# Kernel optimization log

Measured on AMD Instinct MI355X. Metric: run time of the kernel, lower is better.

## Reference

```python
import jax, jax.numpy as jnp
import numpy as np

N = 100_000   # nodes
E = 3_200_000 # edges (avg degree 32)
D = 128       # feature dim
L = 3         # encoder layers (GIN convs)
K = 2         # MLP linear layers per GIN conv (channel_list [128,128,128])
G = 64        # graphs in batch
C = 4         # output classes
BN_EPS = 1e-5


def setup_inputs() -> dict:
    key = jax.random.key(0)
    ks = jax.random.split(key, 12)
    x = jax.random.normal(ks[0], (N, D), dtype=jnp.float32)
    edge_index = jax.random.randint(ks[1], (2, E), 0, N, dtype=jnp.int64)
    batch = jnp.sort(jax.random.randint(ks[2], (N,), 0, G, dtype=jnp.int64))
    # GIN MLP params: L convs x K linear layers each, all D->D
    Ws = jax.random.normal(ks[3], (L, K, D, D), dtype=jnp.float32) * 0.05
    bs = jax.random.normal(ks[4], (L, K, D), dtype=jnp.float32) * 0.02
    # BatchNorm (eval mode) params/buffers per MLP layer
    gammas = 1.0 + 0.1 * jax.random.normal(ks[5], (L, K, D), dtype=jnp.float32)
    betas = 0.1 * jax.random.normal(ks[6], (L, K, D), dtype=jnp.float32)
    run_means = 0.1 * jax.random.normal(ks[7], (L, K, D), dtype=jnp.float32)
    run_vars = jax.random.uniform(ks[8], (L, K, D), dtype=jnp.float32, minval=0.5, maxval=1.5)
    # final classifier
    lin_W = jax.random.normal(ks[9], (D, C), dtype=jnp.float32) * 0.05
    lin_b = jax.random.normal(ks[10], (C,), dtype=jnp.float32) * 0.02
    return {"x": x, "edge_index": edge_index, "batch": batch,
            "Ws": Ws, "bs": bs, "gammas": gammas, "betas": betas,
            "run_means": run_means, "run_vars": run_vars,
            "lin_W": lin_W, "lin_b": lin_b}


def reference(x, edge_index, batch, Ws, bs, gammas, betas, run_means, run_vars, lin_W, lin_b):
    src, dst = edge_index[0], edge_index[1]
    h = x
    for l in range(L):
        # GINConv (eps=0): h_i <- MLP(h_i + sum_{j->i} h_j)
        agg = jax.ops.segment_sum(h[src], dst, num_segments=N)  # [N, D]
        h = h + agg
        for k in range(K):
            # Linear -> BatchNorm(eval) -> ReLU (plain_last=False, dropout=0)
            y = h @ Ws[l, k] + bs[l, k]
            scale = gammas[l, k] / jnp.sqrt(run_vars[l, k] + BN_EPS)
            h = jax.nn.relu((y - run_means[l, k]) * scale + betas[l, k])
    pooled = jax.ops.segment_max(h, batch, num_segments=G)  # [G, D]
    logits = pooled @ lin_W + lin_b                          # [G, C]
    return jax.nn.log_softmax(logits, axis=-1)
```

## Files before the change

### kernel.cpp

```cpp
#include <hip/hip_runtime.h>
#include <stdint.h>

#define NN 100000
#define EE 3200000
#define DD 128
#define GG 64
#define CC 4
#define LLAYERS 3
#define KLIN 2
#define BN_EPS 1e-5f

#define BSH 8
#define NB ((NN + 255) >> BSH)
#define CHUNK3 8192
#define NBLK3 ((EE + CHUNK3 - 1) / CHUNK3)
#define STAGE_CAP 10240

#define HSP 136

typedef unsigned short u16;
typedef unsigned int u32;
typedef short bf16x8 __attribute__((ext_vector_type(8)));
typedef float f32x4 __attribute__((ext_vector_type(4)));

__device__ __forceinline__ float bflo(u32 u){ return __uint_as_float(u << 16); }
__device__ __forceinline__ float bfhi(u32 u){ return __uint_as_float(u & 0xffff0000u); }
__device__ __forceinline__ u16 f2bf(float f){
  u32 u = __float_as_uint(f);
  u32 r = u + 0x7fffu + ((u >> 16) & 1u);
  return (u16)(r >> 16);
}


__global__ __launch_bounds__(256) void bucket_hist(const int* __restrict__ dst,
                                                   int* __restrict__ bcount){
  __shared__ int lh[NB];
  for (int i = threadIdx.x; i < NB; i += 256) lh[i] = 0;
  __syncthreads();
  int b0 = blockIdx.x * CHUNK3;
  int bend = min(b0 + CHUNK3, EE);
  for (int i = b0 + threadIdx.x; i < bend; i += 256)
    atomicAdd(&lh[dst[i] >> BSH], 1);
  __syncthreads();
  for (int i = threadIdx.x; i < NB; i += 256)
    if (lh[i]) atomicAdd(&bcount[i], lh[i]);
}

__global__ __launch_bounds__(512) void bucket_scan(const int* __restrict__ bcount,
                                                   int* __restrict__ bofs,
                                                   int* __restrict__ gcur,
                                                   int* __restrict__ row_start){
  __shared__ int s[512];
  int t = threadIdx.x;
  int v = (t < NB) ? bcount[t] : 0;
  s[t] = v; __syncthreads();
  for (int off = 1; off < 512; off <<= 1) {
    int u = (t >= off) ? s[t - off] : 0;
    __syncthreads();
    s[t] += u;
    __syncthreads();
  }
  if (t < NB) { int e = s[t] - v; bofs[t] = e; gcur[t] = e; }
  if (t == 0) row_start[NN] = EE;
}

__global__ __launch_bounds__(256) void bucket_scatter(const int* __restrict__ src,
                                                      const int* __restrict__ dst,
                                                      int* __restrict__ gcur,
                                                      int2* __restrict__ rec){
  __shared__ int lh[NB];
  __shared__ int lbase[NB];
  int b0 = blockIdx.x * CHUNK3;
  int bend = min(b0 + CHUNK3, EE);
  for (int i = threadIdx.x; i < NB; i += 256) lh[i] = 0;
  __syncthreads();
  for (int i = b0 + threadIdx.x; i < bend; i += 256)
    atomicAdd(&lh[dst[i] >> BSH], 1);
  __syncthreads();
  for (int i = threadIdx.x; i < NB; i += 256) {
    int c = lh[i];
    lbase[i] = c ? atomicAdd(&gcur[i], c) : 0;
    lh[i] = 0;
  }
  __syncthreads();
  for (int i = b0 + threadIdx.x; i < bend; i += 256) {
    int d = dst[i];
    int bk = d >> BSH;
    int pos = lbase[bk] + atomicAdd(&lh[bk], 1);
    rec[pos] = make_int2(src[i], d & ((1 << BSH) - 1));
  }
}

__global__ __launch_bounds__(256) void bucket_emit(const int2* __restrict__ rec,
                                                   const int* __restrict__ bofs,
                                                   const int* __restrict__ bcount,
                                                   int* __restrict__ row_start,
                                                   int* __restrict__ sorted_src){
  __shared__ int cnt[256];
  __shared__ int ofs[256];
  __shared__ int stage[STAGE_CAP];
  const int b = blockIdx.x, t = threadIdx.x;
  const int nodebase = b << BSH;
  const int nlocal = min(256, NN - nodebase);
  const int ebeg = bofs[b];
  const int ecnt = bcount[b];
  cnt[t] = 0;
  __syncthreads();
  for (int i = t; i < ecnt; i += 256) {
    int2 r = rec[ebeg + i];
    atomicAdd(&cnt[r.y], 1);
  }
  __syncthreads();
  int v = cnt[t];
  ofs[t] = v;
  __syncthreads();
  for (int off = 1; off < 256; off <<= 1) {
    int u = (t >= off) ? ofs[t - off] : 0;
    __syncthreads();
    ofs[t] += u;
    __syncthreads();
  }
  int excl = ofs[t] - v;
  if (t < nlocal) row_start[nodebase + t] = ebeg + excl;
  cnt[t] = excl;
  __syncthreads();
  for (int i = t; i < ecnt; i += 256) {
    int2 r = rec[ebeg + i];
    int pos = atomicAdd(&cnt[r.y], 1);
    if (pos < STAGE_CAP) stage[pos] = r.x;
    else sorted_src[ebeg + pos] = r.x;
  }
  __syncthreads();
  int lim = min(ecnt, STAGE_CAP);
  for (int i = t; i < lim; i += 256)
    sorted_src[ebeg + i] = stage[i];
}

__global__ __launch_bounds__(256) void prep_kernel(const float* __restrict__ Ws,
    const float* __restrict__ bs, const float* __restrict__ gammas,
    const float* __restrict__ betas, const float* __restrict__ means,
    const float* __restrict__ vars,
    u16* __restrict__ Wt6, float* __restrict__ scale6, float* __restrict__ shift6){
  const int s = blockIdx.x;
  const float* W = Ws + (size_t)s * DD * DD;
  u16* Wt = Wt6 + (size_t)s * DD * DD;
  const int t = threadIdx.x;
  if (t < DD) {
    float sc = gammas[s*DD+t] * rsqrtf(vars[s*DD+t] + BN_EPS);
    scale6[s*DD+t] = sc;
    shift6[s*DD+t] = (bs[s*DD+t] - means[s*DD+t]) * sc + betas[s*DD+t];
  }
  for (int f = t; f < DD*DD; f += 256) {
    int j = f & 7, lane = (f >> 3) & 63, ks = (f >> 9) & 3, ct = f >> 11;
    int k = ks*32 + (lane >> 4)*8 + j;
    int n = ct*16 + (lane & 15);
    Wt[f] = f2bf(W[k*DD + n]);
  }
}

__global__ __launch_bounds__(256) void cast_x_kernel(const float4* __restrict__ x,
                                                     uint4* __restrict__ h){
  int i = blockIdx.x * 256 + threadIdx.x;
  if (i < NN*DD/8) {
    float4 a = x[2*i], b = x[2*i+1];
    uint4 o;
    o.x = (u32)f2bf(a.x) | ((u32)f2bf(a.y) << 16);
    o.y = (u32)f2bf(a.z) | ((u32)f2bf(a.w) << 16);
    o.z = (u32)f2bf(b.x) | ((u32)f2bf(b.y) << 16);
    o.w = (u32)f2bf(b.z) | ((u32)f2bf(b.w) << 16);
    h[i] = o;
  }
}

__global__ __launch_bounds__(256) void gin_layer(
    const u16* __restrict__ H, u16* __restrict__ O,
    const int* __restrict__ row_start, const int* __restrict__ sorted_src,
    const u16* __restrict__ W1t, const float* __restrict__ scale1, const float* __restrict__ shift1,
    const u16* __restrict__ W2t, const float* __restrict__ scale2, const float* __restrict__ shift2)
{
  __shared__ u16 HS[16][HSP];
  __shared__ u16 YS[16][HSP];

  const int tid = threadIdx.x;
  const int base = blockIdx.x * 16;
  const uint4* hp = (const uint4*)H;

  {
    const int g = tid >> 4, l16 = tid & 15;
    const int node = base + g;
    uint4 v = hp[(size_t)node*16 + l16];
    float a0=bflo(v.x), a1=bfhi(v.x), a2=bflo(v.y), a3=bfhi(v.y);
    float a4=bflo(v.z), a5=bfhi(v.z), a6=bflo(v.w), a7=bfhi(v.w);
    float b0=0.f,b1=0.f,b2=0.f,b3=0.f,b4=0.f,b5=0.f,b6=0.f,b7=0.f;
    float c0=0.f,c1=0.f,c2=0.f,c3=0.f,c4=0.f,c5=0.f,c6=0.f,c7=0.f;
    float d0=0.f,d1=0.f,d2=0.f,d3=0.f,d4=0.f,d5=0.f,d6=0.f,d7=0.f;
    int e = row_start[node];
    const int end = row_start[node + 1];
    for (; e + 3 < end; e += 4) {
      int s0 = sorted_src[e],   s1 = sorted_src[e+1];
      int s2 = sorted_src[e+2], s3 = sorted_src[e+3];
      uint4 u0 = hp[(size_t)s0*16 + l16];
      uint4 u1 = hp[(size_t)s1*16 + l16];
      uint4 u2 = hp[(size_t)s2*16 + l16];
      uint4 u3 = hp[(size_t)s3*16 + l16];
      a0 += bflo(u0.x); a1 += bfhi(u0.x); a2 += bflo(u0.y); a3 += bfhi(u0.y);
      a4 += bflo(u0.z); a5 += bfhi(u0.z); a6 += bflo(u0.w); a7 += bfhi(u0.w);
      b0 += bflo(u1.x); b1 += bfhi(u1.x); b2 += bflo(u1.y); b3 += bfhi(u1.y);
      b4 += bflo(u1.z); b5 += bfhi(u1.z); b6 += bflo(u1.w); b7 += bfhi(u1.w);
      c0 += bflo(u2.x); c1 += bfhi(u2.x); c2 += bflo(u2.y); c3 += bfhi(u2.y);
      c4 += bflo(u2.z); c5 += bfhi(u2.z); c6 += bflo(u2.w); c7 += bfhi(u2.w);
      d0 += bflo(u3.x); d1 += bfhi(u3.x); d2 += bflo(u3.y); d3 += bfhi(u3.y);
      d4 += bflo(u3.z); d5 += bfhi(u3.z); d6 += bflo(u3.w); d7 += bfhi(u3.w);
    }
    for (; e < end; ++e) {
      int s0 = sorted_src[e];
      uint4 u0 = hp[(size_t)s0*16 + l16];
      a0 += bflo(u0.x); a1 += bfhi(u0.x); a2 += bflo(u0.y); a3 += bfhi(u0.y);
      a4 += bflo(u0.z); a5 += bfhi(u0.z); a6 += bflo(u0.w); a7 += bfhi(u0.w);
    }
    a0 += b0+c0+d0; a1 += b1+c1+d1; a2 += b2+c2+d2; a3 += b3+c3+d3;
    a4 += b4+c4+d4; a5 += b5+c5+d5; a6 += b6+c6+d6; a7 += b7+c7+d7;
    uint4 w;
    w.x = (u32)f2bf(a0) | ((u32)f2bf(a1) << 16);
    w.y = (u32)f2bf(a2) | ((u32)f2bf(a3) << 16);
    w.z = (u32)f2bf(a4) | ((u32)f2bf(a5) << 16);
    w.w = (u32)f2bf(a6) | ((u32)f2bf(a7) << 16);
    *(uint4*)&HS[g][l16*8] = w;
  }
  __syncthreads();

  const int wave = tid >> 6, lane = tid & 63;
  const int ln15 = lane & 15, quad = lane >> 4;

  {
    bf16x8 af[4];
    #pragma unroll
    for (int ks = 0; ks < 4; ++ks)
      af[ks] = *(const bf16x8*)&HS[ln15][ks*32 + quad*8];
    f32x4 acc[2];
    acc[0] = (f32x4){0.f,0.f,0.f,0.f};
    acc[1] = (f32x4){0.f,0.f,0.f,0.f};
    #pragma unroll
    for (int ks = 0; ks < 4; ++ks) {
      #pragma unroll
      for (int j = 0; j < 2; ++j) {
        const int ct = wave*2 + j;
        bf16x8 bf = *(const bf16x8*)(W1t + (((ct*4 + ks)*64 + lane) << 3));
        acc[j] = __builtin_amdgcn_mfma_f32_16x16x32_bf16(af[ks], bf, acc[j], 0, 0, 0);
      }
    }
    #pragma unroll
    for (int j = 0; j < 2; ++j) {
      const int col = (wave*2 + j)*16 + ln15;
      const float sc = scale1[col], sh = shift1[col];
      #pragma unroll
      for (int reg = 0; reg < 4; ++reg)
        YS[quad*4 + reg][col] = f2bf(fmaxf(acc[j][reg]*sc + sh, 0.f));
    }
  }
  __syncthreads();

  {
    bf16x8 af[4];
    #pragma unroll
    for (int ks = 0; ks < 4; ++ks)
      af[ks] = *(const bf16x8*)&YS[ln15][ks*32 + quad*8];
    f32x4 acc[2];
    acc[0] = (f32x4){0.f,0.f,0.f,0.f};
    acc[1] = (f32x4){0.f,0.f,0.f,0.f};
    #pragma unroll
    for (int ks = 0; ks < 4; ++ks) {
      #pragma unroll
      for (int j = 0; j < 2; ++j) {
        const int ct = wave*2 + j;
        bf16x8 bf = *(const bf16x8*)(W2t + (((ct*4 + ks)*64 + lane) << 3));
        acc[j] = __builtin_amdgcn_mfma_f32_16x16x32_bf16(af[ks], bf, acc[j], 0, 0, 0);
      }
    }
    #pragma unroll
    for (int j = 0; j < 2; ++j) {
      const int col = (wave*2 + j)*16 + ln15;
      const float sc = scale2[col], sh = shift2[col];
      #pragma unroll
      for (int reg = 0; reg < 4; ++reg) {
        const int row = base + quad*4 + reg;
        O[(size_t)row * DD + col] = f2bf(fmaxf(acc[j][reg]*sc + sh, 0.f));
      }
    }
  }
}

__global__ __launch_bounds__(256) void pool_seg_bf16(const u16* __restrict__ h,
    const int* __restrict__ batch, float* __restrict__ pooled){
  __shared__ float red[256 * 8];
  __shared__ int range[2];
  const int g = blockIdx.x, tid = threadIdx.x;
  if (tid < 2) {
    int target = g + tid;
    int lo = 0, hi = NN;
    while (lo < hi) { int mid = (lo + hi) >> 1; if (batch[mid] < target) lo = mid + 1; else hi = mid; }
    range[tid] = lo;
  }
  __syncthreads();
  const int beg = range[0], end = range[1];
  const int rg = tid >> 4, l16 = tid & 15;
  const uint4* hp = (const uint4*)h;
  float m0=0.f,m1=0.f,m2=0.f,m3=0.f,m4=0.f,m5=0.f,m6=0.f,m7=0.f;
  for (int n = beg + rg; n < end; n += 16) {
    uint4 u = hp[(size_t)n * 16 + l16];
    m0 = fmaxf(m0, bflo(u.x)); m1 = fmaxf(m1, bfhi(u.x));
    m2 = fmaxf(m2, bflo(u.y)); m3 = fmaxf(m3, bfhi(u.y));
    m4 = fmaxf(m4, bflo(u.z)); m5 = fmaxf(m5, bfhi(u.z));
    m6 = fmaxf(m6, bflo(u.w)); m7 = fmaxf(m7, bfhi(u.w));
  }
  float* r = &red[tid * 8];
  r[0]=m0; r[1]=m1; r[2]=m2; r[3]=m3; r[4]=m4; r[5]=m5; r[6]=m6; r[7]=m7;
  __syncthreads();
  #pragma unroll
  for (int off = 8; off > 0; off >>= 1) {
    if (rg < off) {
      float* o = &red[(tid + off*16) * 8];
      #pragma unroll
      for (int i = 0; i < 8; ++i) r[i] = fmaxf(r[i], o[i]);
    }
    __syncthreads();
  }
  if (rg == 0) {
    #pragma unroll
    for (int i = 0; i < 8; ++i) pooled[g*DD + l16*8 + i] = r[i];
  }
}

__global__ __launch_bounds__(64) void classify_kernel(const float* __restrict__ pooled,
    const float* __restrict__ lw, const float* __restrict__ lb, float* __restrict__ out){
  int g = blockIdx.x, lane = threadIdx.x;
  float x0 = pooled[g*DD + lane];
  float x1 = pooled[g*DD + 64 + lane];
  float4 wA = *(const float4*)(lw + lane*4);
  float4 wB = *(const float4*)(lw + (lane+64)*4);
  float a0 = x0*wA.x + x1*wB.x;
  float a1 = x0*wA.y + x1*wB.y;
  float a2 = x0*wA.z + x1*wB.z;
  float a3 = x0*wA.w + x1*wB.w;
  #pragma unroll
  for (int off = 32; off > 0; off >>= 1) {
    a0 += __shfl_down(a0, off);
    a1 += __shfl_down(a1, off);
    a2 += __shfl_down(a2, off);
    a3 += __shfl_down(a3, off);
  }
  if (lane == 0) {
    float l0 = a0 + lb[0];
    float l1 = a1 + lb[1];
    float l2 = a2 + lb[2];
    float l3 = a3 + lb[3];
    float m = fmaxf(fmaxf(l0,l1), fmaxf(l2,l3));
    float s = expf(l0-m)+expf(l1-m)+expf(l2-m)+expf(l3-m);
    float lse = logf(s) + m;
    out[g*4+0] = l0 - lse;
    out[g*4+1] = l1 - lse;
    out[g*4+2] = l2 - lse;
    out[g*4+3] = l3 - lse;
  }
}

extern "C" void kernel_launch(void* const* d_in, const int* in_sizes, int n_in,
                              void* d_out, int out_size, void* d_ws, size_t ws_size,
                              hipStream_t stream) {
  const float* x     = (const float*)d_in[0];
  const int* ei      = (const int*)d_in[1];
  const int* batch   = (const int*)d_in[2];
  const float* Ws    = (const float*)d_in[3];
  const float* bs    = (const float*)d_in[4];
  const float* gammas= (const float*)d_in[5];
  const float* betas = (const float*)d_in[6];
  const float* means = (const float*)d_in[7];
  const float* vars  = (const float*)d_in[8];
  const float* lw    = (const float*)d_in[9];
  const float* lb    = (const float*)d_in[10];
  float* out = (float*)d_out;

  u16* hA = (u16*)d_ws;
  u16* hB = hA + (size_t)NN * DD;
  float* pooled = (float*)(hB + (size_t)NN * DD);
  float* scale6 = pooled + GG * DD;
  float* shift6 = scale6 + 6 * DD;
  int* row_start  = (int*)(shift6 + 6 * DD);
  int* bcount     = row_start + NN + 2;
  int* bofs       = bcount + NB;
  int* gcur       = bofs + NB;
  int* sorted_src = gcur + NB + 3;
  u16* Wt6 = (u16*)(((uintptr_t)(sorted_src + EE) + 63) & ~(uintptr_t)63);
  int2* rec = (int2*)hA;

  const int* srcIdx = ei;
  const int* dstIdx = ei + EE;

  hipMemsetAsync(bcount, 0, NB * sizeof(int), stream);
  bucket_hist<<<NBLK3, 256, 0, stream>>>(dstIdx, bcount);
  bucket_scan<<<1, 512, 0, stream>>>(bcount, bofs, gcur, row_start);
  bucket_scatter<<<NBLK3, 256, 0, stream>>>(srcIdx, dstIdx, gcur, rec);
  bucket_emit<<<NB, 256, 0, stream>>>(rec, bofs, bcount, row_start, sorted_src);

  prep_kernel<<<6, 256, 0, stream>>>(Ws, bs, gammas, betas, means, vars,
                                     Wt6, scale6, shift6);
  cast_x_kernel<<<(NN*DD/8 + 255)/256, 256, 0, stream>>>((const float4*)x, (uint4*)hA);

  u16* cur = hA;
  u16* tmp = hB;
  const int layer_grid = NN / 16;
  for (int l = 0; l < LLAYERS; ++l) {
    int s0 = l*KLIN + 0, s1 = l*KLIN + 1;
    gin_layer<<<layer_grid, 256, 0, stream>>>(cur, tmp, row_start, sorted_src,
        Wt6 + (size_t)s0*DD*DD, scale6 + s0*DD, shift6 + s0*DD,
        Wt6 + (size_t)s1*DD*DD, scale6 + s1*DD, shift6 + s1*DD);
    u16* t = cur; cur = tmp; tmp = t;
  }

  pool_seg_bf16<<<GG, 256, 0, stream>>>(cur, batch, pooled);
  classify_kernel<<<GG, 64, 0, stream>>>(pooled, lw, lb, out);
}
```

Baseline: 650.4 us.

## Pack edge records, vectorize bucketing loads, fuse prep/cast and pool/classify

Edge records in the bucketing sort are packed from an int2 into a single u32 (src shifted left by 8, local dst in the low byte), halving the rec traffic in scatter and emit. The histogram and scatter loops now read src and dst as int4 vectors. The weight-prep and x-cast kernels are merged into one launch, and segment-max pooling is fused with the classifier, which removes two launches and the pooled buffer. Packing assumes src fits in 24 bits, which holds for N=100000.

```diff
diff --git a/kernel.cpp b/kernel.cpp
--- a/kernel.cpp
+++ b/kernel.cpp
@@ -37,10 +37,19 @@
   __shared__ int lh[NB];
   for (int i = threadIdx.x; i < NB; i += 256) lh[i] = 0;
   __syncthreads();
-  int b0 = blockIdx.x * CHUNK3;
-  int bend = min(b0 + CHUNK3, EE);
-  for (int i = b0 + threadIdx.x; i < bend; i += 256)
-    atomicAdd(&lh[dst[i] >> BSH], 1);
+  const int b0 = blockIdx.x * CHUNK3;
+  const int cnt = min(CHUNK3, EE - b0);
+  const int4* d4 = (const int4*)(dst + b0);
+  const int n4 = cnt >> 2;
+  for (int i = threadIdx.x; i < n4; i += 256) {
+    int4 v = d4[i];
+    atomicAdd(&lh[v.x >> BSH], 1);
+    atomicAdd(&lh[v.y >> BSH], 1);
+    atomicAdd(&lh[v.z >> BSH], 1);
+    atomicAdd(&lh[v.w >> BSH], 1);
+  }
+  for (int i = (n4 << 2) + threadIdx.x; i < cnt; i += 256)
+    atomicAdd(&lh[dst[b0 + i] >> BSH], 1);
   __syncthreads();
   for (int i = threadIdx.x; i < NB; i += 256)
     if (lh[i]) atomicAdd(&bcount[i], lh[i]);
@@ -67,15 +76,25 @@
 __global__ __launch_bounds__(256) void bucket_scatter(const int* __restrict__ src,
                                                       const int* __restrict__ dst,
                                                       int* __restrict__ gcur,
-                                                      int2* __restrict__ rec){
+                                                      u32* __restrict__ rec){
   __shared__ int lh[NB];
   __shared__ int lbase[NB];
-  int b0 = blockIdx.x * CHUNK3;
-  int bend = min(b0 + CHUNK3, EE);
+  const int b0 = blockIdx.x * CHUNK3;
+  const int cnt = min(CHUNK3, EE - b0);
+  const int n4 = cnt >> 2;
+  const int4* s4 = (const int4*)(src + b0);
+  const int4* d4 = (const int4*)(dst + b0);
   for (int i = threadIdx.x; i < NB; i += 256) lh[i] = 0;
   __syncthreads();
-  for (int i = b0 + threadIdx.x; i < bend; i += 256)
-    atomicAdd(&lh[dst[i] >> BSH], 1);
+  for (int i = threadIdx.x; i < n4; i += 256) {
+    int4 v = d4[i];
+    atomicAdd(&lh[v.x >> BSH], 1);
+    atomicAdd(&lh[v.y >> BSH], 1);
+    atomicAdd(&lh[v.z >> BSH], 1);
+    atomicAdd(&lh[v.w >> BSH], 1);
+  }
+  for (int i = (n4 << 2) + threadIdx.x; i < cnt; i += 256)
+    atomicAdd(&lh[dst[b0 + i] >> BSH], 1);
   __syncthreads();
   for (int i = threadIdx.x; i < NB; i += 256) {
     int c = lh[i];
@@ -83,15 +102,38 @@
     lh[i] = 0;
   }
   __syncthreads();
-  for (int i = b0 + threadIdx.x; i < bend; i += 256) {
-    int d = dst[i];
+  for (int i = threadIdx.x; i < n4; i += 256) {
+    int4 ss = s4[i], dd = d4[i];
+    {
+      int bk = dd.x >> BSH;
+      int pos = lbase[bk] + atomicAdd(&lh[bk], 1);
+      rec[pos] = ((u32)ss.x << BSH) | (u32)(dd.x & 255);
+    }
+    {
+      int bk = dd.y >> BSH;
+      int pos = lbase[bk] + atomicAdd(&lh[bk], 1);
+      rec[pos] = ((u32)ss.y << BSH) | (u32)(dd.y & 255);
+    }
+    {
+      int bk = dd.z >> BSH;
+      int pos = lbase[bk] + atomicAdd(&lh[bk], 1);
+      rec[pos] = ((u32)ss.z << BSH) | (u32)(dd.z & 255);
+    }
+    {
+      int bk = dd.w >> BSH;
+      int pos = lbase[bk] + atomicAdd(&lh[bk], 1);
+      rec[pos] = ((u32)ss.w << BSH) | (u32)(dd.w & 255);
+    }
+  }
+  for (int i = (n4 << 2) + threadIdx.x; i < cnt; i += 256) {
+    int d = dst[b0 + i];
     int bk = d >> BSH;
     int pos = lbase[bk] + atomicAdd(&lh[bk], 1);
-    rec[pos] = make_int2(src[i], d & ((1 << BSH) - 1));
-  }
-}
-
-__global__ __launch_bounds__(256) void bucket_emit(const int2* __restrict__ rec,
+    rec[pos] = ((u32)src[b0 + i] << BSH) | (u32)(d & 255);
+  }
+}
+
+__global__ __launch_bounds__(256) void bucket_emit(const u32* __restrict__ rec,
                                                    const int* __restrict__ bofs,
                                                    const int* __restrict__ bcount,
                                                    int* __restrict__ row_start,
@@ -106,10 +148,8 @@
   const int ecnt = bcount[b];
   cnt[t] = 0;
   __syncthreads();
-  for (int i = t; i < ecnt; i += 256) {
-    int2 r = rec[ebeg + i];
-    atomicAdd(&cnt[r.y], 1);
-  }
+  for (int i = t; i < ecnt; i += 256)
+    atomicAdd(&cnt[rec[ebeg + i] & 255u], 1);
   __syncthreads();
   int v = cnt[t];
   ofs[t] = v;
@@ -125,10 +165,10 @@
   cnt[t] = excl;
   __syncthreads();
   for (int i = t; i < ecnt; i += 256) {
-    int2 r = rec[ebeg + i];
-    int pos = atomicAdd(&cnt[r.y], 1);
-    if (pos < STAGE_CAP) stage[pos] = r.x;
-    else sorted_src[ebeg + pos] = r.x;
+    u32 r = rec[ebeg + i];
+    int pos = atomicAdd(&cnt[r & 255u], 1);
+    if (pos < STAGE_CAP) stage[pos] = (int)(r >> BSH);
+    else sorted_src[ebeg + pos] = (int)(r >> BSH);
   }
   __syncthreads();
   int lim = min(ecnt, STAGE_CAP);
@@ -136,39 +176,39 @@
     sorted_src[ebeg + i] = stage[i];
 }
 
-__global__ __launch_bounds__(256) void prep_kernel(const float* __restrict__ Ws,
+__global__ __launch_bounds__(256) void prep_cast_kernel(const float* __restrict__ Ws,
     const float* __restrict__ bs, const float* __restrict__ gammas,
     const float* __restrict__ betas, const float* __restrict__ means,
     const float* __restrict__ vars,
-    u16* __restrict__ Wt6, float* __restrict__ scale6, float* __restrict__ shift6){
-  const int s = blockIdx.x;
-  const float* W = Ws + (size_t)s * DD * DD;
-  u16* Wt = Wt6 + (size_t)s * DD * DD;
-  const int t = threadIdx.x;
-  if (t < DD) {
-    float sc = gammas[s*DD+t] * rsqrtf(vars[s*DD+t] + BN_EPS);
-    scale6[s*DD+t] = sc;
-    shift6[s*DD+t] = (bs[s*DD+t] - means[s*DD+t]) * sc + betas[s*DD+t];
-  }
-  for (int f = t; f < DD*DD; f += 256) {
-    int j = f & 7, lane = (f >> 3) & 63, ks = (f >> 9) & 3, ct = f >> 11;
-    int k = ks*32 + (lane >> 4)*8 + j;
-    int n = ct*16 + (lane & 15);
-    Wt[f] = f2bf(W[k*DD + n]);
-  }
-}
-
-__global__ __launch_bounds__(256) void cast_x_kernel(const float4* __restrict__ x,
-                                                     uint4* __restrict__ h){
-  int i = blockIdx.x * 256 + threadIdx.x;
-  if (i < NN*DD/8) {
-    float4 a = x[2*i], b = x[2*i+1];
-    uint4 o;
-    o.x = (u32)f2bf(a.x) | ((u32)f2bf(a.y) << 16);
-    o.y = (u32)f2bf(a.z) | ((u32)f2bf(a.w) << 16);
-    o.z = (u32)f2bf(b.x) | ((u32)f2bf(b.y) << 16);
-    o.w = (u32)f2bf(b.z) | ((u32)f2bf(b.w) << 16);
-    h[i] = o;
+    u16* __restrict__ Wt6, float* __restrict__ scale6, float* __restrict__ shift6,
+    const float4* __restrict__ x, uint4* __restrict__ h){
+  if (blockIdx.x < 6) {
+    const int s = blockIdx.x;
+    const float* W = Ws + (size_t)s * DD * DD;
+    u16* Wt = Wt6 + (size_t)s * DD * DD;
+    const int t = threadIdx.x;
+    if (t < DD) {
+      float sc = gammas[s*DD+t] * rsqrtf(vars[s*DD+t] + BN_EPS);
+      scale6[s*DD+t] = sc;
+      shift6[s*DD+t] = (bs[s*DD+t] - means[s*DD+t]) * sc + betas[s*DD+t];
+    }
+    for (int f = t; f < DD*DD; f += 256) {
+      int j = f & 7, lane = (f >> 3) & 63, ks = (f >> 9) & 3, ct = f >> 11;
+      int k = ks*32 + (lane >> 4)*8 + j;
+      int n = ct*16 + (lane & 15);
+      Wt[f] = f2bf(W[k*DD + n]);
+    }
+  } else {
+    int i = (blockIdx.x - 6) * 256 + threadIdx.x;
+    if (i < NN*DD/8) {
+      float4 a = x[2*i], b = x[2*i+1];
+      uint4 o;
+      o.x = (u32)f2bf(a.x) | ((u32)f2bf(a.y) << 16);
+      o.y = (u32)f2bf(a.z) | ((u32)f2bf(a.w) << 16);
+      o.z = (u32)f2bf(b.x) | ((u32)f2bf(b.y) << 16);
+      o.w = (u32)f2bf(b.z) | ((u32)f2bf(b.w) << 16);
+      h[i] = o;
+    }
   }
 }
 
@@ -290,9 +330,11 @@
   }
 }
 
-__global__ __launch_bounds__(256) void pool_seg_bf16(const u16* __restrict__ h,
-    const int* __restrict__ batch, float* __restrict__ pooled){
+__global__ __launch_bounds__(256) void pool_classify(const u16* __restrict__ h,
+    const int* __restrict__ batch, const float* __restrict__ lw,
+    const float* __restrict__ lb, float* __restrict__ out){
   __shared__ float red[256 * 8];
+  __shared__ float P[DD];
   __shared__ int range[2];
   const int g = blockIdx.x, tid = threadIdx.x;
   if (tid < 2) {
@@ -327,40 +369,38 @@
   }
   if (rg == 0) {
     #pragma unroll
-    for (int i = 0; i < 8; ++i) pooled[g*DD + l16*8 + i] = r[i];
-  }
-}
-
-__global__ __launch_bounds__(64) void classify_kernel(const float* __restrict__ pooled,
-    const float* __restrict__ lw, const float* __restrict__ lb, float* __restrict__ out){
-  int g = blockIdx.x, lane = threadIdx.x;
-  float x0 = pooled[g*DD + lane];
-  float x1 = pooled[g*DD + 64 + lane];
-  float4 wA = *(const float4*)(lw + lane*4);
-  float4 wB = *(const float4*)(lw + (lane+64)*4);
-  float a0 = x0*wA.x + x1*wB.x;
-  float a1 = x0*wA.y + x1*wB.y;
-  float a2 = x0*wA.z + x1*wB.z;
-  float a3 = x0*wA.w + x1*wB.w;
-  #pragma unroll
-  for (int off = 32; off > 0; off >>= 1) {
-    a0 += __shfl_down(a0, off);
-    a1 += __shfl_down(a1, off);
-    a2 += __shfl_down(a2, off);
-    a3 += __shfl_down(a3, off);
-  }
-  if (lane == 0) {
-    float l0 = a0 + lb[0];
-    float l1 = a1 + lb[1];
-    float l2 = a2 + lb[2];
-    float l3 = a3 + lb[3];
-    float m = fmaxf(fmaxf(l0,l1), fmaxf(l2,l3));
-    float s = expf(l0-m)+expf(l1-m)+expf(l2-m)+expf(l3-m);
-    float lse = logf(s) + m;
-    out[g*4+0] = l0 - lse;
-    out[g*4+1] = l1 - lse;
-    out[g*4+2] = l2 - lse;
-    out[g*4+3] = l3 - lse;
+    for (int i = 0; i < 8; ++i) P[l16*8 + i] = r[i];
+  }
+  __syncthreads();
+  if (tid < 64) {
+    float x0 = P[tid];
+    float x1 = P[tid + 64];
+    float4 wA = *(const float4*)(lw + tid*4);
+    float4 wB = *(const float4*)(lw + (tid+64)*4);
+    float a0 = x0*wA.x + x1*wB.x;
+    float a1 = x0*wA.y + x1*wB.y;
+    float a2 = x0*wA.z + x1*wB.z;
+    float a3 = x0*wA.w + x1*wB.w;
+    #pragma unroll
+    for (int off = 32; off > 0; off >>= 1) {
+      a0 += __shfl_down(a0, off);
+      a1 += __shfl_down(a1, off);
+      a2 += __shfl_down(a2, off);
+      a3 += __shfl_down(a3, off);
+    }
+    if (tid == 0) {
+      float l0 = a0 + lb[0];
+      float l1 = a1 + lb[1];
+      float l2 = a2 + lb[2];
+      float l3 = a3 + lb[3];
+      float m = fmaxf(fmaxf(l0,l1), fmaxf(l2,l3));
+      float s = expf(l0-m)+expf(l1-m)+expf(l2-m)+expf(l3-m);
+      float lse = logf(s) + m;
+      out[g*4+0] = l0 - lse;
+      out[g*4+1] = l1 - lse;
+      out[g*4+2] = l2 - lse;
+      out[g*4+3] = l3 - lse;
+    }
   }
 }
 
@@ -382,8 +422,7 @@
 
   u16* hA = (u16*)d_ws;
   u16* hB = hA + (size_t)NN * DD;
-  float* pooled = (float*)(hB + (size_t)NN * DD);
-  float* scale6 = pooled + GG * DD;
+  float* scale6 = (float*)(hB + (size_t)NN * DD);
   float* shift6 = scale6 + 6 * DD;
   int* row_start  = (int*)(shift6 + 6 * DD);
   int* bcount     = row_start + NN + 2;
@@ -391,7 +430,7 @@
   int* gcur       = bofs + NB;
   int* sorted_src = gcur + NB + 3;
   u16* Wt6 = (u16*)(((uintptr_t)(sorted_src + EE) + 63) & ~(uintptr_t)63);
-  int2* rec = (int2*)hA;
+  u32* rec = (u32*)hA;
 
   const int* srcIdx = ei;
   const int* dstIdx = ei + EE;
@@ -402,9 +441,9 @@
   bucket_scatter<<<NBLK3, 256, 0, stream>>>(srcIdx, dstIdx, gcur, rec);
   bucket_emit<<<NB, 256, 0, stream>>>(rec, bofs, bcount, row_start, sorted_src);
 
-  prep_kernel<<<6, 256, 0, stream>>>(Ws, bs, gammas, betas, means, vars,
-                                     Wt6, scale6, shift6);
-  cast_x_kernel<<<(NN*DD/8 + 255)/256, 256, 0, stream>>>((const float4*)x, (uint4*)hA);
+  prep_cast_kernel<<<6 + (NN*DD/8 + 255)/256, 256, 0, stream>>>(
+      Ws, bs, gammas, betas, means, vars, Wt6, scale6, shift6,
+      (const float4*)x, (uint4*)hA);
 
   u16* cur = hA;
   u16* tmp = hB;
@@ -417,6 +456,5 @@
     u16* t = cur; cur = tmp; tmp = t;
   }
 
-  pool_seg_bf16<<<GG, 256, 0, stream>>>(cur, batch, pooled);
-  classify_kernel<<<GG, 64, 0, stream>>>(pooled, lw, lb, out);
-}
+  pool_classify<<<GG, 256, 0, stream>>>(cur, batch, lw, lb, out);
+}
```

New measurement: 612.4 us (median of 2 runs). 1.06x faster.
